# Performance work log

Hardware: AMD Instinct MI355X
Metric: run time of the kernel (lower is better)

The kernel has to match this reference:

```python
import jax, jax.numpy as jnp
import numpy as np

B, P, T = 32, 196, 32           # batch, num pixels (14*14), seq_len
E, H, A, V = 512, 512, 256, 30000  # embed, hidden, attention, vocab
FEAT = 2048

def _ln(x, g, b, eps=1e-5):
    m = jnp.mean(x, -1, keepdims=True)
    v = jnp.mean((x - m) ** 2, -1, keepdims=True)
    return (x - m) / jnp.sqrt(v + eps) * g + b

def setup_inputs() -> dict:
    key = jax.random.key(0)
    ks = iter(jax.random.split(key, 32))
    def rn(shape, s=0.05):
        return (jax.random.normal(next(ks), shape, dtype=jnp.float32) * s)
    inp = {
        'features': jax.random.normal(next(ks), (B, P, FEAT), dtype=jnp.float32),
        'captions': jax.random.randint(next(ks), (B, T), 0, V),
        # feature adapter Linear(2048->E) + LayerNorm
        'Wad': rn((E, FEAT)), 'bad': jnp.zeros((E,), jnp.float32),
        'g_ad': jnp.ones((E,), jnp.float32), 'b_ad': jnp.zeros((E,), jnp.float32),
        # additive attention
        'We': rn((A, E)), 'be': jnp.zeros((A,), jnp.float32),
        'Wd': rn((A, H)), 'bd': jnp.zeros((A,), jnp.float32),
        'Wf': rn((1, A)), 'bf': jnp.zeros((1,), jnp.float32),
        # embedding table (uniform(-0.1,0.1) as in torch init)
        'emb': jax.random.uniform(next(ks), (V, E), jnp.float32, -0.1, 0.1),
        # LSTM layer 0: input 2E, layer 1: input H; gates order i,f,g,o; forget bias 1
        'W_ih0': rn((4 * H, 2 * E)), 'W_hh0': rn((4 * H, H)),
        'b_ih0': jnp.concatenate([jnp.zeros(H), jnp.ones(H), jnp.zeros(2 * H)]).astype(jnp.float32),
        'b_hh0': jnp.zeros((4 * H,), jnp.float32),
        'W_ih1': rn((4 * H, H)), 'W_hh1': rn((4 * H, H)),
        'b_ih1': jnp.concatenate([jnp.zeros(H), jnp.ones(H), jnp.zeros(2 * H)]).astype(jnp.float32),
        'b_hh1': jnp.zeros((4 * H,), jnp.float32),
        # output head
        'W1': rn((H // 2, H)), 'b1': jnp.zeros((H // 2,), jnp.float32),
        'g1': jnp.ones((H // 2,), jnp.float32), 'bb1': jnp.zeros((H // 2,), jnp.float32),
        'W2': rn((V, H // 2)), 'b2': jnp.zeros((V,), jnp.float32),
    }
    return inp

def reference(features, captions, Wad, bad, g_ad, b_ad, We, be, Wd, bd, Wf, bf,
              emb, W_ih0, W_hh0, b_ih0, b_hh0, W_ih1, W_hh1, b_ih1, b_hh1,
              W1, b1, g1, bb1, W2, b2):
    # feature adapter (dropout = identity in eval)
    enc = _ln(jax.nn.relu(features @ Wad.T + bad), g_ad, b_ad)   # [B,P,E]
    att1 = enc @ We.T + be                                        # [B,P,A] (same every step)
    embs = emb[captions]                                          # [B,T,E]

    def lstm_cell(x, h, c, Wih, Whh, bih, bhh):
        gates = x @ Wih.T + bih + h @ Whh.T + bhh                 # [B,4H]
        i, f, g, o = jnp.split(gates, 4, axis=1)
        c_n = jax.nn.sigmoid(f) * c + jax.nn.sigmoid(i) * jnp.tanh(g)
        h_n = jax.nn.sigmoid(o) * jnp.tanh(c_n)
        return h_n, c_n

    def step(carry, emb_t):
        h, c = carry                                              # each [2,B,H]
        # additive attention against top-layer hidden state
        att2 = h[1] @ Wd.T + bd                                   # [B,A]
        e = (jax.nn.relu(att1 + att2[:, None, :]) @ Wf.T + bf)[..., 0]  # [B,P]
        alpha = jax.nn.softmax(e, axis=1)                         # (max-subtract is folded in)
        ctx = jnp.einsum('bp,bpe->be', alpha, enc)                # [B,E]
        x = jnp.concatenate([emb_t, ctx], axis=1)                 # [B,2E]
        h0, c0 = lstm_cell(x,  h[0], c[0], W_ih0, W_hh0, b_ih0, b_hh0)
        h1, c1 = lstm_cell(h0, h[1], c[1], W_ih1, W_hh1, b_ih1, b_hh1)
        out = jax.nn.relu(_ln(h1 @ W1.T + b1, g1, bb1))
        out = jnp.clip(out @ W2.T + b2, -10.0, 10.0)              # [B,V]
        return (jnp.stack([h0, h1]), jnp.stack([c0, c1])), out

    h0 = jnp.zeros((2, B, H), jnp.float32)
    c0 = jnp.zeros((2, B, H), jnp.float32)
    _, outs = jax.lax.scan(step, (h0, c0), jnp.swapaxes(embs, 0, 1))
    return jnp.swapaxes(outs, 0, 1)                               # [B,T,V]
```

## Files before the change

kernel.cpp:

```cpp
#include <hip/hip_runtime.h>

#define B_ 32
#define P_ 196
#define T_ 32
#define E_ 512
#define H_ 512
#define A_ 256
#define V_ 30000
#define FEAT_ 2048

typedef unsigned short u16;
typedef __attribute__((ext_vector_type(8))) short bf16x8;
typedef __attribute__((ext_vector_type(4))) float fx4;

#define MFMA16 __builtin_amdgcn_mfma_f32_16x16x32_bf16

__device__ __forceinline__ u16 f2b(float f){
  unsigned u = __builtin_bit_cast(unsigned, f);
  u += 0x7FFFu + ((u >> 16) & 1u);
  return (u16)(u >> 16);
}
__device__ __forceinline__ float b2f(u16 h){
  unsigned u = ((unsigned)h) << 16;
  return __builtin_bit_cast(float, u);
}
__device__ __forceinline__ float sigm(float x){ return 1.f/(1.f + __expf(-x)); }

__global__ void k_convert(const float* __restrict__ src, u16* __restrict__ dst, int n8){
  int i = blockIdx.x*256 + threadIdx.x;
  if (i >= n8) return;
  const float4* s = (const float4*)src + (size_t)i*2;
  float4 a = s[0], b = s[1];
  ushort4* d = (ushort4*)dst + (size_t)i*2;
  d[0] = make_ushort4(f2b(a.x), f2b(a.y), f2b(a.z), f2b(a.w));
  d[1] = make_ushort4(f2b(b.x), f2b(b.y), f2b(b.z), f2b(b.w));
}

__global__ void k_gather(const float* __restrict__ emb, const int* __restrict__ cap,
                         u16* __restrict__ dst){
  int r = blockIdx.x, l = threadIdx.x;
  int t = r >> 5, b = r & 31;
  int c = cap[b*T_ + t];
  const float4* s = (const float4*)(emb + (size_t)c*E_) + l*2;
  float4 a = s[0], bb = s[1];
  ushort4* d = (ushort4*)(dst + (size_t)r*E_) + l*2;
  d[0] = make_ushort4(f2b(a.x), f2b(a.y), f2b(a.z), f2b(a.w));
  d[1] = make_ushort4(f2b(bb.x), f2b(bb.y), f2b(bb.z), f2b(bb.w));
}

__global__ void k_pack_wd2(const float* __restrict__ Wd, unsigned* __restrict__ dst){
  int i = blockIdx.x*256 + threadIdx.x;
  if (i >= 256*256) return;
  int n = i & 255, kp = i >> 8;
  unsigned lo = f2b(Wd[n*512 + 2*kp]);
  unsigned hi = f2b(Wd[n*512 + 2*kp + 1]);
  dst[i] = lo | (hi << 16);
}

__global__ void k_pack_g0(const float* __restrict__ Wih, const float* __restrict__ Whh,
                          u16* __restrict__ dst){
  int eid = blockIdx.x*256 + threadIdx.x;
  if (eid >= 6144*512) return;
  int j = eid & 7, l = (eid >> 3) & 63, frag = eid >> 9;
  int ks = frag % 12; int rest = frag / 12;
  int kw = rest & 3, q = (rest >> 2) & 3, s = rest >> 4;
  int n = q*512 + s*16 + (l & 15);
  int k = kw*384 + ks*32 + ((l >> 4) << 3) + j;
  float v = (k < 1024) ? Wih[(size_t)n*1024 + k] : Whh[(size_t)n*512 + (k - 1024)];
  dst[eid] = f2b(v);
}

__global__ void k_pack_w1p(const float* __restrict__ Wih, const float* __restrict__ Whh,
                           u16* __restrict__ dst){
  int eid = blockIdx.x*256 + threadIdx.x;
  if (eid >= 32*128*512) return;
  int j = eid & 7, l = (eid >> 3) & 63, f = eid >> 9;
  int nf = f & 127, s = f >> 7;
  int np = nf*16 + (l & 15);
  int k = ((l >> 4) << 3) + j;
  int orig = ((np >> 4) & 3)*512 + (np >> 6)*16 + (np & 15);
  float v = (k < 16) ? Wih[(size_t)orig*512 + s*16 + k]
                     : Whh[(size_t)orig*512 + s*16 + (k - 16)];
  dst[eid] = f2b(v);
}

__global__ void k_bias_pack(const float* __restrict__ bih, const float* __restrict__ bhh,
                            float* __restrict__ dst){
  int n = blockIdx.x*256 + threadIdx.x;
  if (n >= 2048) return;
  int c = n & 15, q = (n >> 4) & 3, s = n >> 6;
  int orig = q*512 + s*16 + c;
  dst[n] = bih[orig] + bhh[orig];
}

__global__ void k_pack_w2(const float* __restrict__ W2f, u16* __restrict__ W2pk){
  int i = blockIdx.x*256 + threadIdx.x;
  if (i >= 960000) return;
  int l = i & 63, kc = (i >> 6) & 7, nf = i >> 9;
  int row = nf*16 + (l & 15);
  int col = kc*32 + (l >> 4)*8;
  const float4* s = (const float4*)(W2f + (size_t)row*256 + col);
  float4 a = s[0], b = s[1];
  ushort4* d = (ushort4*)(W2pk + (size_t)i*8);
  d[0] = make_ushort4(f2b(a.x), f2b(a.y), f2b(a.z), f2b(a.w));
  d[1] = make_ushort4(f2b(b.x), f2b(b.y), f2b(b.z), f2b(b.w));
}

template<int MODE, int BM, int BN, int KS>
__launch_bounds__(256)
__global__ void k_gemm(const u16* __restrict__ A, const u16* __restrict__ W,
                       const float* __restrict__ bias, u16* __restrict__ outB,
                       int M, int N, int K){
  constexpr int NI = BN/32, MI = BM/32, SEGS = KS/8;
  __shared__ __align__(16) u16 As[BM][KS+8];
  __shared__ __align__(16) u16 Bs[BN][KS+8];
  int tid = threadIdx.x;
  int l = tid & 63, w = tid >> 6;
  int wr = w >> 1, wc = w & 1;
  int m0 = blockIdx.y * BM, n0 = blockIdx.x * BN;
  fx4 acc[MI][NI];
  #pragma unroll
  for (int i=0;i<MI;i++)
    #pragma unroll
    for (int j=0;j<NI;j++) acc[i][j] = (fx4){0.f,0.f,0.f,0.f};
  int lr = l & 15, lg = l >> 4;
  for (int k0 = 0; k0 < K; k0 += KS){
    #pragma unroll
    for (int it=0; it<BM*SEGS/256; ++it){
      int flat = it*256 + tid, rr = flat/SEGS, cs = (flat%SEGS)*8;
      *(uint4*)&As[rr][cs] = *(const uint4*)(A + (size_t)(m0+rr)*K + k0 + cs);
    }
    uint4 z = {0u,0u,0u,0u};
    #pragma unroll
    for (int it=0; it<BN*SEGS/256; ++it){
      int flat = it*256 + tid, rr = flat/SEGS, cs = (flat%SEGS)*8;
      int rb = n0 + rr;
      *(uint4*)&Bs[rr][cs] = (rb < N) ? *(const uint4*)(W + (size_t)rb*K + k0 + cs) : z;
    }
    __syncthreads();
    #pragma unroll
    for (int kk=0; kk<KS/32; ++kk){
      bf16x8 av[MI], bv[NI];
      #pragma unroll
      for (int mi=0; mi<MI; mi++) av[mi] = *(const bf16x8*)&As[wr*(BM/2) + mi*16 + lr][kk*32 + lg*8];
      #pragma unroll
      for (int ni=0; ni<NI; ni++) bv[ni] = *(const bf16x8*)&Bs[wc*(BN/2) + ni*16 + lr][kk*32 + lg*8];
      #pragma unroll
      for (int mi=0; mi<MI; mi++)
        #pragma unroll
        for (int ni=0; ni<NI; ni++)
          acc[mi][ni] = MFMA16(av[mi], bv[ni], acc[mi][ni], 0, 0, 0);
    }
    __syncthreads();
  }
  #pragma unroll
  for (int mi=0; mi<MI; mi++)
    #pragma unroll
    for (int ni=0; ni<NI; ni++){
      int col = n0 + wc*(BN/2) + ni*16 + lr;
      if (col >= N) continue;
      float bvs = bias[col];
      #pragma unroll
      for (int reg=0; reg<4; reg++){
        int rowm = m0 + wr*(BM/2) + mi*16 + lg*4 + reg;
        float v = acc[mi][ni][reg] + bvs;
        if (MODE == 0) v = fmaxf(v, 0.f);
        outB[(size_t)rowm*N + col] = f2b(v);
      }
    }
}

template<int BM, int BN, int KS>
__launch_bounds__(256)
__global__ void k_gemmF(const float* __restrict__ A, const u16* __restrict__ W,
                        const float* __restrict__ bias, u16* __restrict__ outB,
                        int M, int N, int K){
  constexpr int NI = BN/32, MI = BM/32, SEGS = KS/8;
  __shared__ __align__(16) u16 As[BM][KS+8];
  __shared__ __align__(16) u16 Bs[BN][KS+8];
  int tid = threadIdx.x;
  int l = tid & 63, w = tid >> 6;
  int wr = w >> 1, wc = w & 1;
  int m0 = blockIdx.y * BM, n0 = blockIdx.x * BN;
  fx4 acc[MI][NI];
  #pragma unroll
  for (int i=0;i<MI;i++)
    #pragma unroll
    for (int j=0;j<NI;j++) acc[i][j] = (fx4){0.f,0.f,0.f,0.f};
  int lr = l & 15, lg = l >> 4;
  for (int k0 = 0; k0 < K; k0 += KS){
    #pragma unroll
    for (int it=0; it<BM*SEGS/256; ++it){
      int flat = it*256 + tid, rr = flat/SEGS, cs = (flat%SEGS)*8;
      const float4* s = (const float4*)(A + (size_t)(m0+rr)*K + k0 + cs);
      float4 a0 = s[0], a1 = s[1];
      *(ushort4*)&As[rr][cs]   = make_ushort4(f2b(a0.x), f2b(a0.y), f2b(a0.z), f2b(a0.w));
      *(ushort4*)&As[rr][cs+4] = make_ushort4(f2b(a1.x), f2b(a1.y), f2b(a1.z), f2b(a1.w));
    }
    #pragma unroll
    for (int it=0; it<BN*SEGS/256; ++it){
      int flat = it*256 + tid, rr = flat/SEGS, cs = (flat%SEGS)*8;
      *(uint4*)&Bs[rr][cs] = *(const uint4*)(W + (size_t)(n0+rr)*K + k0 + cs);
    }
    __syncthreads();
    #pragma unroll
    for (int kk=0; kk<KS/32; ++kk){
      bf16x8 av[MI], bv[NI];
      #pragma unroll
      for (int mi=0; mi<MI; mi++) av[mi] = *(const bf16x8*)&As[wr*(BM/2) + mi*16 + lr][kk*32 + lg*8];
      #pragma unroll
      for (int ni=0; ni<NI; ni++) bv[ni] = *(const bf16x8*)&Bs[wc*(BN/2) + ni*16 + lr][kk*32 + lg*8];
      #pragma unroll
      for (int mi=0; mi<MI; mi++)
        #pragma unroll
        for (int ni=0; ni<NI; ni++)
          acc[mi][ni] = MFMA16(av[mi], bv[ni], acc[mi][ni], 0, 0, 0);
    }
    __syncthreads();
  }
  #pragma unroll
  for (int mi=0; mi<MI; mi++)
    #pragma unroll
    for (int ni=0; ni<NI; ni++){
      int col = n0 + wc*(BN/2) + ni*16 + lr;
      float bvs = bias[col];
      #pragma unroll
      for (int reg=0; reg<4; reg++){
        int rowm = m0 + wr*(BM/2) + mi*16 + lg*4 + reg;
        float v = fmaxf(acc[mi][ni][reg] + bvs, 0.f);
        outB[(size_t)rowm*N + col] = f2b(v);
      }
    }
}

__global__ void k_ln1(const u16* __restrict__ pre, const float* __restrict__ g,
                      const float* __restrict__ bt, u16* __restrict__ enc){
  int row = blockIdx.x; int l = threadIdx.x;
  bf16x8 vv = *(const bf16x8*)(pre + (size_t)row*E_ + l*8);
  float x[8]; float s = 0.f;
  #pragma unroll
  for (int i=0;i<8;i++){ x[i] = b2f((u16)vv[i]); s += x[i]; }
  #pragma unroll
  for (int off=32; off; off>>=1) s += __shfl_xor(s, off, 64);
  float mean = s * (1.f/512.f);
  float vs = 0.f;
  #pragma unroll
  for (int i=0;i<8;i++){ float d = x[i]-mean; vs += d*d; }
  #pragma unroll
  for (int off=32; off; off>>=1) vs += __shfl_xor(vs, off, 64);
  float inv = rsqrtf(vs*(1.f/512.f) + 1e-5f);
  int c0 = l*8;
  u16 o[8];
  #pragma unroll
  for (int i=0;i<8;i++) o[i] = f2b((x[i]-mean)*inv*g[c0+i] + bt[c0+i]);
  ushort4* d = (ushort4*)(enc + (size_t)row*E_ + c0);
  d[0] = make_ushort4(o[0],o[1],o[2],o[3]);
  d[1] = make_ushort4(o[4],o[5],o[6],o[7]);
}

__device__ __forceinline__ void w1ln_block(const u16* __restrict__ h1all,
    const u16* __restrict__ W1, const float* __restrict__ b1,
    const float* __restrict__ g1v, const float* __restrict__ bb1,
    u16* __restrict__ hid, int u, int tid, float* red2, float* mv){
  int l = tid & 63, w = tid >> 6, lr = l & 15, lg = l >> 4;
  fx4 acc[2] = {{0,0,0,0},{0,0,0,0}};
  for (int k0 = 0; k0 < 512; k0 += 32){
    bf16x8 bv  = *(const bf16x8*)(W1 + (size_t)(w*16+lr)*512 + k0 + lg*8);
    bf16x8 av0 = *(const bf16x8*)(h1all + ((size_t)lr*T_ + u)*512 + k0 + lg*8);
    bf16x8 av1 = *(const bf16x8*)(h1all + ((size_t)(16+lr)*T_ + u)*512 + k0 + lg*8);
    acc[0] = MFMA16(av0, bv, acc[0], 0,0,0);
    acc[1] = MFMA16(av1, bv, acc[1], 0,0,0);
  }
  int col = w*16 + lr;
  float bc = b1[col];
  float val[2][4], s1[2][4], s2[2][4];
  #pragma unroll
  for (int mi=0;mi<2;mi++)
    #pragma unroll
    for (int reg=0;reg<4;reg++){
      float v = acc[mi][reg] + bc;
      val[mi][reg] = v; s1[mi][reg] = v; s2[mi][reg] = v*v;
    }
  #pragma unroll
  for (int off=1; off<16; off<<=1){
    #pragma unroll
    for (int mi=0;mi<2;mi++)
      #pragma unroll
      for (int reg=0;reg<4;reg++){
        s1[mi][reg] += __shfl_xor(s1[mi][reg], off, 64);
        s2[mi][reg] += __shfl_xor(s2[mi][reg], off, 64);
      }
  }
  if (lr == 0){
    #pragma unroll
    for (int mi=0;mi<2;mi++)
      #pragma unroll
      for (int reg=0;reg<4;reg++){
        int row = mi*16 + lg*4 + reg;
        red2[(0*16 + w)*32 + row] = s1[mi][reg];
        red2[(16   + w)*32 + row] = s2[mi][reg];
      }
  }
  __syncthreads();
  if (tid < 64){
    int which = tid >> 5, row = tid & 31;
    float s = 0.f;
    #pragma unroll
    for (int ww=0; ww<16; ++ww) s += red2[(which*16 + ww)*32 + row];
    mv[which*32 + row] = s;
  }
  __syncthreads();
  #pragma unroll
  for (int mi=0;mi<2;mi++)
    #pragma unroll
    for (int reg=0;reg<4;reg++){
      int row = mi*16 + lg*4 + reg;
      float mean = mv[row] * (1.f/256.f);
      float var  = mv[32+row] * (1.f/256.f) - mean*mean;
      float inv  = rsqrtf(var + 1e-5f);
      float o = fmaxf((val[mi][reg]-mean)*inv*g1v[col] + bb1[col], 0.f);
      hid[((size_t)u*32 + row)*256 + col] = f2b(o);
    }
}

__launch_bounds__(1024)
__global__ void k_w1(const u16* __restrict__ h1all, const u16* __restrict__ W1_16,
                     const float* __restrict__ b1, const float* __restrict__ g1v,
                     const float* __restrict__ bb1, u16* __restrict__ hid16){
  __shared__ float red2[1024];
  __shared__ float mv[64];
  w1ln_block(h1all, W1_16, b1, g1v, bb1, hid16, blockIdx.x, threadIdx.x, red2, mv);
}

__launch_bounds__(1024)
__global__ void k_head(const u16* __restrict__ hid, const u16* __restrict__ W2pk,
                       const float* __restrict__ b2, float* __restrict__ out){
  __shared__ __align__(16) union { u16 hA[32][264]; float Cs[32][260]; } S;
  int c = blockIdx.x, uh = blockIdx.y, tid = threadIdx.x;
  int l = tid & 63, w = tid >> 6, lr = l & 15, lg = l >> 4;
  int nf = c*16 + w;
  bool valid = nf < 1875;
  bf16x8 bw[8];
  if (valid){
    const u16* wp = W2pk + (size_t)nf*4096 + l*8;
    #pragma unroll
    for (int k0=0;k0<8;k0++) bw[k0] = *(const bf16x8*)(wp + k0*512);
  }
  int srow = tid >> 5, scc = (tid & 31)*8;
  int col0 = c*256 + scc;
  float bb[8];
  #pragma unroll
  for (int j=0;j<8;j++) bb[j] = (col0 + j < V_) ? b2[col0 + j] : 0.f;

  for (int ui=0; ui<16; ++ui){
    int u = uh*16 + ui;
    { int arow = tid >> 5, ak = (tid & 31)*8;
      *(uint4*)&S.hA[arow][ak] = *(const uint4*)(hid + ((size_t)u*32 + arow)*256 + ak); }
    __syncthreads();
    fx4 acc0 = {0,0,0,0}, acc1 = {0,0,0,0};
    if (valid){
      #pragma unroll
      for (int k0=0;k0<8;k0++){
        bf16x8 av0 = *(const bf16x8*)&S.hA[lr][k0*32 + lg*8];
        bf16x8 av1 = *(const bf16x8*)&S.hA[16+lr][k0*32 + lg*8];
        acc0 = MFMA16(av0, bw[k0], acc0, 0,0,0);
        acc1 = MFMA16(av1, bw[k0], acc1, 0,0,0);
      }
    }
    __syncthreads();
    #pragma unroll
    for (int reg=0; reg<4; ++reg){
      S.Cs[lg*4+reg][w*16+lr]    = acc0[reg];
      S.Cs[16+lg*4+reg][w*16+lr] = acc1[reg];
    }
    __syncthreads();
    if (col0 + 8 <= V_){
      float4 v0, v1;
      v0.x = fminf(fmaxf(S.Cs[srow][scc+0] + bb[0], -10.f), 10.f);
      v0.y = fminf(fmaxf(S.Cs[srow][scc+1] + bb[1], -10.f), 10.f);
      v0.z = fminf(fmaxf(S.Cs[srow][scc+2] + bb[2], -10.f), 10.f);
      v0.w = fminf(fmaxf(S.Cs[srow][scc+3] + bb[3], -10.f), 10.f);
      v1.x = fminf(fmaxf(S.Cs[srow][scc+4] + bb[4], -10.f), 10.f);
      v1.y = fminf(fmaxf(S.Cs[srow][scc+5] + bb[5], -10.f), 10.f);
      v1.z = fminf(fmaxf(S.Cs[srow][scc+6] + bb[6], -10.f), 10.f);
      v1.w = fminf(fmaxf(S.Cs[srow][scc+7] + bb[7], -10.f), 10.f);
      float* o = out + ((size_t)srow*T_ + u)*V_ + col0;
      *(float4*)o = v0; *(float4*)(o+4) = v1;
    }
    __syncthreads();
  }
}

__launch_bounds__(1024)
__global__ void k_ly(const float* __restrict__ part1, const float* __restrict__ bias1p,
                     float* __restrict__ c1buf, u16* __restrict__ h1all,
                     const unsigned* __restrict__ Wd2, const float* __restrict__ bd,
                     const u16* __restrict__ att1b, const u16* __restrict__ enc16,
                     const float* __restrict__ Wf, const float* __restrict__ bfp,
                     const u16* __restrict__ embs, u16* __restrict__ xh0cur, int t){
  int b = blockIdx.x, tid = threadIdx.x;
  int l = tid & 63, wid = tid >> 6;
  __shared__ float g1s[2048];
  __shared__ float h1s[512];
  __shared__ float a2p[4][256];
  __shared__ float a2[256], ev[256], red[8], wfv[256], bdv[256];
  __shared__ float cb[4][256][2];
  if (tid < 256){ wfv[tid] = Wf[tid]; bdv[tid] = bd[tid]; }
  float bf0 = bfp[0];

  if (t > 0){
    float acc0 = bias1p[tid], acc1 = bias1p[tid + 1024];
    #pragma unroll 4
    for (int s2=0; s2<32; ++s2){
      const float* pp = part1 + ((size_t)(s2*32 + b))*2048;
      acc0 += pp[tid];
      acc1 += pp[tid + 1024];
    }
    g1s[tid] = acc0; g1s[tid + 1024] = acc1;
    __syncthreads();
    if (tid < 512){
      int h = tid, s4 = h >> 4, c = h & 15, base = s4*64 + c;
      float gi = g1s[base], gf = g1s[base+16], gg = g1s[base+32], go = g1s[base+48];
      float cold = c1buf[b*512 + h];
      float cn = sigm(gf)*cold + sigm(gi)*tanhf(gg);
      c1buf[b*512 + h] = cn;
      float hn = sigm(go)*tanhf(cn);
      h1s[h] = hn;
      h1all[((size_t)b*T_ + (t-1))*512 + h] = f2b(hn);
    }
  } else {
    if (tid < 512) h1s[tid] = 0.f;
  }
  __syncthreads();
  if (t >= T_) return;

  {
    int n = tid & 255, kq = tid >> 8;
    float acc = 0.f;
    const unsigned* wp = Wd2 + (size_t)kq*64*256 + n;
    #pragma unroll 8
    for (int kp2 = 0; kp2 < 64; ++kp2){
      unsigned wv = wp[(size_t)kp2*256];
      int k0 = (kq*64 + kp2)*2;
      acc += h1s[k0]   * b2f((u16)(wv & 0xFFFFu))
           + h1s[k0+1] * b2f((u16)(wv >> 16));
    }
    a2p[kq][n] = acc;
  }
  __syncthreads();
  if (tid < 256) a2[tid] = a2p[0][tid] + a2p[1][tid] + a2p[2][tid] + a2p[3][tid] + bdv[tid];
  __syncthreads();
  for (int pi = 0; pi < 13; ++pi){
    int p = pi*16 + wid;
    if (p < P_){
      ushort4 av4 = *(const ushort4*)(att1b + (size_t)(b*P_ + p)*A_ + l*4);
      int j0 = l*4;
      float sum = fmaxf(b2f(av4.x)+a2[j0],  0.f)*wfv[j0]
                + fmaxf(b2f(av4.y)+a2[j0+1],0.f)*wfv[j0+1]
                + fmaxf(b2f(av4.z)+a2[j0+2],0.f)*wfv[j0+2]
                + fmaxf(b2f(av4.w)+a2[j0+3],0.f)*wfv[j0+3];
      #pragma unroll
      for (int off=32; off; off>>=1) sum += __shfl_xor(sum, off, 64);
      if (l == 0) ev[p] = sum + bf0;
    }
  }
  __syncthreads();
  if (tid < 256){
    float v = (tid < P_) ? ev[tid] : -1e30f;
    float m = v;
    #pragma unroll
    for (int off=32; off; off>>=1) m = fmaxf(m, __shfl_xor(m, off, 64));
    if (l == 0) red[wid] = m;
  }
  __syncthreads();
  float mg = fmaxf(fmaxf(red[0],red[1]), fmaxf(red[2],red[3]));
  if (tid < 256){
    float ex = (tid < P_) ? __expf(ev[tid] - mg) : 0.f;
    float ss = ex;
    #pragma unroll
    for (int off=32; off; off>>=1) ss += __shfl_xor(ss, off, 64);
    if (l == 0) red[4+wid] = ss;
    ev[tid] = ex;
  }
  __syncthreads();
  float inv = 1.f/(red[4]+red[5]+red[6]+red[7]);
  {
    int j = tid & 255, pq = tid >> 8;
    float A0 = 0.f, A1 = 0.f;
    const unsigned* ep = (const unsigned*)enc16 + ((size_t)b*P_ + pq*49)*256 + j;
    #pragma unroll 7
    for (int pi = 0; pi < 49; ++pi){
      unsigned vv = ep[(size_t)pi*256];
      float al = ev[pq*49 + pi];
      A0 += al * b2f((u16)(vv & 0xFFFFu));
      A1 += al * b2f((u16)(vv >> 16));
    }
    cb[pq][j][0] = A0; cb[pq][j][1] = A1;
  }
  __syncthreads();
  if (tid < 256){
    float c0 = (cb[0][tid][0]+cb[1][tid][0]+cb[2][tid][0]+cb[3][tid][0]) * inv;
    float c1 = (cb[0][tid][1]+cb[1][tid][1]+cb[2][tid][1]+cb[3][tid][1]) * inv;
    unsigned o = (unsigned)f2b(c0) | (((unsigned)f2b(c1)) << 16);
    *((unsigned*)(xh0cur + (size_t)b*1536 + 512) + tid) = o;
    ((unsigned*)(xh0cur + (size_t)b*1536))[tid] =
        ((const unsigned*)(embs + (size_t)(t*32+b)*E_))[tid];
  }
}

__launch_bounds__(1024)
__global__ void k_lx(const u16* __restrict__ xh0cur, u16* __restrict__ xh0nxt,
                     const u16* __restrict__ Wg0pk, const float* __restrict__ bias0p,
                     const u16* __restrict__ W1ppk, const u16* __restrict__ h1all,
                     float* __restrict__ c0buf, float* __restrict__ part1, int t){
  __shared__ float part[16][32][16];
  __shared__ float gsum[4][32][16];
  __shared__ __align__(16) u16 As[32][40];
  int tid = threadIdx.x, s = blockIdx.x;
  int l = tid & 63, kw = tid >> 6, lr = l & 15, lg = l >> 4;

  bf16x8 a[2][3];
  #pragma unroll
  for (int mi=0;mi<2;mi++)
    #pragma unroll
    for (int ks=0;ks<3;ks++)
      a[mi][ks] = *(const bf16x8*)(xh0cur + (size_t)(mi*16+lr)*1536 + kw*96 + ks*32 + lg*8);
  for (int q=0;q<4;q++){
    fx4 acc0 = (fx4){0,0,0,0}, acc1 = (fx4){0,0,0,0};
    const u16* wp = Wg0pk + (size_t)(((s*4+q)*4 + (kw>>2))*12 + (kw&3)*3)*512 + l*8;
    #pragma unroll
    for (int ks=0;ks<3;ks++){
      bf16x8 bf8 = *(const bf16x8*)(wp + ks*512);
      acc0 = MFMA16(a[0][ks], bf8, acc0, 0,0,0);
      acc1 = MFMA16(a[1][ks], bf8, acc1, 0,0,0);
    }
    #pragma unroll
    for (int reg=0;reg<4;reg++){
      part[kw][lg*4+reg][lr]    = acc0[reg];
      part[kw][16+lg*4+reg][lr] = acc1[reg];
    }
    __syncthreads();
    if (tid < 512){
      int bb = tid >> 4, c = tid & 15;
      float g = bias0p[s*64 + q*16 + c];
      #pragma unroll
      for (int kw2=0; kw2<16; ++kw2) g += part[kw2][bb][c];
      gsum[q][bb][c] = g;
    }
    __syncthreads();
  }
  if (tid < 256){
    int bb = tid >> 3, kk = (tid & 7)*2;
    unsigned hv = 0;
    if (t > 0) hv = *(const unsigned*)(h1all + ((size_t)bb*T_ + (t-1))*512 + s*16 + kk);
    *(unsigned*)&As[bb][16+kk] = hv;
  }
  if (tid < 512){
    int bb = tid >> 4, c = tid & 15;
    int h = s*16 + c;
    float gi = gsum[0][bb][c], gf = gsum[1][bb][c], gg = gsum[2][bb][c], go = gsum[3][bb][c];
    float cold = c0buf[bb*512 + h];
    float cn = sigm(gf)*cold + sigm(gi)*tanhf(gg);
    c0buf[bb*512 + h] = cn;
    u16 hb = f2b(sigm(go)*tanhf(cn));
    xh0nxt[(size_t)bb*1536 + 1024 + h] = hb;
    As[bb][c] = hb;
  }
  __syncthreads();
  bf16x8 pa0 = *(const bf16x8*)&As[lr][lg*8];
  bf16x8 pa1 = *(const bf16x8*)&As[16+lr][lg*8];
  #pragma unroll 2
  for (int i=0;i<8;i++){
    int nf = kw*8 + i;
    bf16x8 bf8 = *(const bf16x8*)(W1ppk + (size_t)(s*128 + nf)*512 + l*8);
    fx4 A0 = MFMA16(pa0, bf8, (fx4){0,0,0,0}, 0,0,0);
    fx4 A1 = MFMA16(pa1, bf8, (fx4){0,0,0,0}, 0,0,0);
    float* o = part1 + ((size_t)s*32)*2048 + nf*16 + lr;
    #pragma unroll
    for (int reg=0;reg<4;reg++){
      o[(size_t)(lg*4+reg)*2048]    = A0[reg];
      o[(size_t)(16+lg*4+reg)*2048] = A1[reg];
    }
  }
}

extern "C" void kernel_launch(void* const* d_in, const int* in_sizes, int n_in,
                              void* d_out, int out_size, void* d_ws, size_t ws_size,
                              hipStream_t stream){
  (void)in_sizes; (void)n_in; (void)out_size; (void)ws_size;
  const float* features = (const float*)d_in[0];
  const int*   captions = (const int*)d_in[1];
  const float* Wad  = (const float*)d_in[2];
  const float* bad  = (const float*)d_in[3];
  const float* g_ad = (const float*)d_in[4];
  const float* b_ad = (const float*)d_in[5];
  const float* We   = (const float*)d_in[6];
  const float* be   = (const float*)d_in[7];
  const float* Wd   = (const float*)d_in[8];
  const float* bd   = (const float*)d_in[9];
  const float* Wf   = (const float*)d_in[10];
  const float* bfp  = (const float*)d_in[11];
  const float* emb  = (const float*)d_in[12];
  const float* W_ih0 = (const float*)d_in[13];
  const float* W_hh0 = (const float*)d_in[14];
  const float* b_ih0 = (const float*)d_in[15];
  const float* b_hh0 = (const float*)d_in[16];
  const float* W_ih1 = (const float*)d_in[17];
  const float* W_hh1 = (const float*)d_in[18];
  const float* b_ih1 = (const float*)d_in[19];
  const float* b_hh1 = (const float*)d_in[20];
  const float* W1  = (const float*)d_in[21];
  const float* b1  = (const float*)d_in[22];
  const float* g1  = (const float*)d_in[23];
  const float* bb1 = (const float*)d_in[24];
  const float* W2  = (const float*)d_in[25];
  const float* b2  = (const float*)d_in[26];
  float* out = (float*)d_out;

  char* wsb = (char*)d_ws;
  size_t off = 0;
  auto alloc = [&](size_t bytes)->char*{
    char* p = wsb + off; off += (bytes + 255) & ~(size_t)255; return p;
  };
  u16* Wad16   = (u16*)alloc((size_t)512*2048*2);
  u16* We16    = (u16*)alloc((size_t)256*512*2);
  u16* W1_16   = (u16*)alloc((size_t)256*512*2);
  u16* W2pk    = (u16*)alloc((size_t)1875*8*512*2);
  unsigned* Wd2 = (unsigned*)alloc((size_t)256*256*4);
  u16* Wg0pk   = (u16*)alloc((size_t)2048*1536*2);
  u16* W1ppk   = (u16*)alloc((size_t)32*128*512*2);
  float* bias0p = (float*)alloc(2048*4);
  float* bias1p = (float*)alloc(2048*4);
  u16* embs16  = (u16*)alloc((size_t)1024*512*2);
  u16* pre16   = (u16*)alloc((size_t)6272*512*2);
  u16* enc16   = (u16*)alloc((size_t)6272*512*2);
  u16* att1_16 = (u16*)alloc((size_t)6272*256*2);
  u16* xh0     = (u16*)alloc((size_t)2*32*1536*2);
  float* c0buf = (float*)alloc(32*512*4);
  float* c1buf = (float*)alloc(32*512*4);
  float* part1 = (float*)alloc((size_t)32*32*2048*4);
  u16* h1all16 = (u16*)alloc((size_t)1024*512*2);
  u16* hid16   = (u16*)alloc((size_t)1024*256*2);

  auto cdiv = [](int a, int b){ return (a+b-1)/b; };

  hipMemsetAsync(xh0, 0, 196608 + 65536 + 65536, stream);

  k_convert<<<cdiv(512*2048/8,256),256,0,stream>>>(Wad, Wad16, 512*2048/8);
  k_convert<<<cdiv(256*512/8,256),256,0,stream>>>(We, We16, 256*512/8);
  k_convert<<<cdiv(256*512/8,256),256,0,stream>>>(W1, W1_16, 256*512/8);
  k_pack_w2<<<cdiv(960000,256),256,0,stream>>>(W2, W2pk);
  k_pack_wd2<<<cdiv(256*256,256),256,0,stream>>>(Wd, Wd2);
  k_pack_g0<<<cdiv(6144*512,256),256,0,stream>>>(W_ih0, W_hh0, Wg0pk);
  k_pack_w1p<<<cdiv(32*128*512,256),256,0,stream>>>(W_ih1, W_hh1, W1ppk);
  k_bias_pack<<<8,256,0,stream>>>(b_ih0, b_hh0, bias0p);
  k_bias_pack<<<8,256,0,stream>>>(b_ih1, b_hh1, bias1p);
  k_gather<<<1024,64,0,stream>>>(emb, captions, embs16);

  k_gemmF<64,64,64><<<dim3(8,98),256,0,stream>>>(features, Wad16, bad, pre16, 6272, 512, 2048);
  k_ln1<<<6272,64,0,stream>>>(pre16, g_ad, b_ad, enc16);
  k_gemm<1,64,64,64><<<dim3(4,98),256,0,stream>>>(enc16, We16, be, att1_16, 6272, 256, 512);

  u16* xb[2] = { xh0, xh0 + 32*1536 };
  for (int t = 0; t < T_; ++t){
    k_ly<<<32,1024,0,stream>>>(part1, bias1p, c1buf, h1all16, Wd2, bd,
                               att1_16, enc16, Wf, bfp, embs16, xb[t&1], t);
    k_lx<<<32,1024,0,stream>>>(xb[t&1], xb[1-(t&1)], Wg0pk, bias0p,
                               W1ppk, h1all16, c0buf, part1, t);
  }
  k_ly<<<32,1024,0,stream>>>(part1, bias1p, c1buf, h1all16, Wd2, bd,
                             att1_16, enc16, Wf, bfp, embs16, xb[0], T_);

  k_w1<<<32,1024,0,stream>>>(h1all16, W1_16, b1, g1, bb1, hid16);
  k_head<<<dim3(118,2),1024,0,stream>>>(hid16, W2pk, b2, out);
}
```

Measured before the change: 1.367 ms.

## Merge prep kernels, swizzle GEMM block order, restructure layer-0 gate reduction

```diff
diff --git a/kernel.cpp b/kernel.cpp
--- a/kernel.cpp
+++ b/kernel.cpp
@@ -26,87 +26,100 @@
 }
 __device__ __forceinline__ float sigm(float x){ return 1.f/(1.f + __expf(-x)); }
 
-__global__ void k_convert(const float* __restrict__ src, u16* __restrict__ dst, int n8){
-  int i = blockIdx.x*256 + threadIdx.x;
-  if (i >= n8) return;
-  const float4* s = (const float4*)src + (size_t)i*2;
-  float4 a = s[0], b = s[1];
-  ushort4* d = (ushort4*)dst + (size_t)i*2;
-  d[0] = make_ushort4(f2b(a.x), f2b(a.y), f2b(a.z), f2b(a.w));
-  d[1] = make_ushort4(f2b(b.x), f2b(b.y), f2b(b.z), f2b(b.w));
-}
-
-__global__ void k_gather(const float* __restrict__ emb, const int* __restrict__ cap,
-                         u16* __restrict__ dst){
-  int r = blockIdx.x, l = threadIdx.x;
-  int t = r >> 5, b = r & 31;
-  int c = cap[b*T_ + t];
-  const float4* s = (const float4*)(emb + (size_t)c*E_) + l*2;
-  float4 a = s[0], bb = s[1];
-  ushort4* d = (ushort4*)(dst + (size_t)r*E_) + l*2;
-  d[0] = make_ushort4(f2b(a.x), f2b(a.y), f2b(a.z), f2b(a.w));
-  d[1] = make_ushort4(f2b(bb.x), f2b(bb.y), f2b(bb.z), f2b(bb.w));
-}
-
-__global__ void k_pack_wd2(const float* __restrict__ Wd, unsigned* __restrict__ dst){
-  int i = blockIdx.x*256 + threadIdx.x;
-  if (i >= 256*256) return;
-  int n = i & 255, kp = i >> 8;
-  unsigned lo = f2b(Wd[n*512 + 2*kp]);
-  unsigned hi = f2b(Wd[n*512 + 2*kp + 1]);
-  dst[i] = lo | (hi << 16);
-}
-
-__global__ void k_pack_g0(const float* __restrict__ Wih, const float* __restrict__ Whh,
-                          u16* __restrict__ dst){
-  int eid = blockIdx.x*256 + threadIdx.x;
-  if (eid >= 6144*512) return;
-  int j = eid & 7, l = (eid >> 3) & 63, frag = eid >> 9;
-  int ks = frag % 12; int rest = frag / 12;
-  int kw = rest & 3, q = (rest >> 2) & 3, s = rest >> 4;
-  int n = q*512 + s*16 + (l & 15);
-  int k = kw*384 + ks*32 + ((l >> 4) << 3) + j;
-  float v = (k < 1024) ? Wih[(size_t)n*1024 + k] : Whh[(size_t)n*512 + (k - 1024)];
-  dst[eid] = f2b(v);
-}
-
-__global__ void k_pack_w1p(const float* __restrict__ Wih, const float* __restrict__ Whh,
-                           u16* __restrict__ dst){
-  int eid = blockIdx.x*256 + threadIdx.x;
-  if (eid >= 32*128*512) return;
-  int j = eid & 7, l = (eid >> 3) & 63, f = eid >> 9;
-  int nf = f & 127, s = f >> 7;
-  int np = nf*16 + (l & 15);
-  int k = ((l >> 4) << 3) + j;
-  int orig = ((np >> 4) & 3)*512 + (np >> 6)*16 + (np & 15);
-  float v = (k < 16) ? Wih[(size_t)orig*512 + s*16 + k]
-                     : Whh[(size_t)orig*512 + s*16 + (k - 16)];
-  dst[eid] = f2b(v);
-}
-
-__global__ void k_bias_pack(const float* __restrict__ bih, const float* __restrict__ bhh,
-                            float* __restrict__ dst){
-  int n = blockIdx.x*256 + threadIdx.x;
-  if (n >= 2048) return;
-  int c = n & 15, q = (n >> 4) & 3, s = n >> 6;
-  int orig = q*512 + s*16 + c;
-  dst[n] = bih[orig] + bhh[orig];
-}
-
-__global__ void k_pack_w2(const float* __restrict__ W2f, u16* __restrict__ W2pk){
-  int i = blockIdx.x*256 + threadIdx.x;
-  if (i >= 960000) return;
-  int l = i & 63, kc = (i >> 6) & 7, nf = i >> 9;
-  int row = nf*16 + (l & 15);
-  int col = kc*32 + (l >> 4)*8;
-  const float4* s = (const float4*)(W2f + (size_t)row*256 + col);
-  float4 a = s[0], b = s[1];
-  ushort4* d = (ushort4*)(W2pk + (size_t)i*8);
-  d[0] = make_ushort4(f2b(a.x), f2b(a.y), f2b(a.z), f2b(a.w));
-  d[1] = make_ushort4(f2b(b.x), f2b(b.y), f2b(b.z), f2b(b.w));
-}
-
-template<int MODE, int BM, int BN, int KS>
+#define PREP_BLOCKS 25398
+__global__ void k_prep(const float* __restrict__ Wad, const float* __restrict__ We,
+                       const float* __restrict__ W1f, const float* __restrict__ W2f,
+                       const float* __restrict__ Wd,
+                       const float* __restrict__ Wih0, const float* __restrict__ Whh0,
+                       const float* __restrict__ Wih1, const float* __restrict__ Whh1,
+                       const float* __restrict__ bih0, const float* __restrict__ bhh0,
+                       const float* __restrict__ bih1, const float* __restrict__ bhh1,
+                       const float* __restrict__ emb, const int* __restrict__ cap,
+                       u16* __restrict__ Wad16, u16* __restrict__ We16,
+                       u16* __restrict__ W1_16, u16* __restrict__ W2pk,
+                       unsigned* __restrict__ Wd2, u16* __restrict__ Wg0pk,
+                       u16* __restrict__ W1ppk, float* __restrict__ bias0p,
+                       float* __restrict__ bias1p, u16* __restrict__ embs16){
+  int bid = blockIdx.x, tid = threadIdx.x;
+  if (bid < 12288){
+    int eid = bid*256 + tid;
+    int j = eid & 7, l = (eid >> 3) & 63, frag = eid >> 9;
+    int ks = frag % 12; int rest = frag / 12;
+    int kw = rest & 3, q = (rest >> 2) & 3, s = rest >> 4;
+    int n = q*512 + s*16 + (l & 15);
+    int k = kw*384 + ks*32 + ((l >> 4) << 3) + j;
+    float v = (k < 1024) ? Wih0[(size_t)n*1024 + k] : Whh0[(size_t)n*512 + (k - 1024)];
+    Wg0pk[eid] = f2b(v);
+  } else if (bid < 20480){
+    int eid = (bid-12288)*256 + tid;
+    int j = eid & 7, l = (eid >> 3) & 63, f = eid >> 9;
+    int nf = f & 127, s = f >> 7;
+    int np = nf*16 + (l & 15);
+    int k = ((l >> 4) << 3) + j;
+    int orig = ((np >> 4) & 3)*512 + (np >> 6)*16 + (np & 15);
+    float v = (k < 16) ? Wih1[(size_t)orig*512 + s*16 + k]
+                       : Whh1[(size_t)orig*512 + s*16 + (k - 16)];
+    W1ppk[eid] = f2b(v);
+  } else if (bid < 24230){
+    int i = (bid-20480)*256 + tid;
+    int l = i & 63, kc = (i >> 6) & 7, nf = i >> 9;
+    int row = nf*16 + (l & 15);
+    int col = kc*32 + (l >> 4)*8;
+    const float4* s = (const float4*)(W2f + (size_t)row*256 + col);
+    float4 a = s[0], b = s[1];
+    ushort4* d = (ushort4*)(W2pk + (size_t)i*8);
+    d[0] = make_ushort4(f2b(a.x), f2b(a.y), f2b(a.z), f2b(a.w));
+    d[1] = make_ushort4(f2b(b.x), f2b(b.y), f2b(b.z), f2b(b.w));
+  } else if (bid < 24742){
+    int i = (bid-24230)*256 + tid;
+    const float4* s = (const float4*)Wad + (size_t)i*2;
+    float4 a = s[0], b = s[1];
+    ushort4* d = (ushort4*)Wad16 + (size_t)i*2;
+    d[0] = make_ushort4(f2b(a.x), f2b(a.y), f2b(a.z), f2b(a.w));
+    d[1] = make_ushort4(f2b(b.x), f2b(b.y), f2b(b.z), f2b(b.w));
+  } else if (bid < 24806){
+    int i = (bid-24742)*256 + tid;
+    const float4* s = (const float4*)We + (size_t)i*2;
+    float4 a = s[0], b = s[1];
+    ushort4* d = (ushort4*)We16 + (size_t)i*2;
+    d[0] = make_ushort4(f2b(a.x), f2b(a.y), f2b(a.z), f2b(a.w));
+    d[1] = make_ushort4(f2b(b.x), f2b(b.y), f2b(b.z), f2b(b.w));
+  } else if (bid < 24870){
+    int i = (bid-24806)*256 + tid;
+    const float4* s = (const float4*)W1f + (size_t)i*2;
+    float4 a = s[0], b = s[1];
+    ushort4* d = (ushort4*)W1_16 + (size_t)i*2;
+    d[0] = make_ushort4(f2b(a.x), f2b(a.y), f2b(a.z), f2b(a.w));
+    d[1] = make_ushort4(f2b(b.x), f2b(b.y), f2b(b.z), f2b(b.w));
+  } else if (bid < 25126){
+    int i = (bid-24870)*256 + tid;
+    int n = i & 255, kp = i >> 8;
+    unsigned lo = f2b(Wd[n*512 + 2*kp]);
+    unsigned hi = f2b(Wd[n*512 + 2*kp + 1]);
+    Wd2[i] = lo | (hi << 16);
+  } else if (bid < 25134){
+    int n = (bid-25126)*256 + tid;
+    int c = n & 15, q = (n >> 4) & 3, s = n >> 6;
+    int orig = q*512 + s*16 + c;
+    bias0p[n] = bih0[orig] + bhh0[orig];
+  } else if (bid < 25142){
+    int n = (bid-25134)*256 + tid;
+    int c = n & 15, q = (n >> 4) & 3, s = n >> 6;
+    int orig = q*512 + s*16 + c;
+    bias1p[n] = bih1[orig] + bhh1[orig];
+  } else {
+    int r = (bid-25142)*4 + (tid >> 6), l = tid & 63;
+    int t = r >> 5, b = r & 31;
+    int c = cap[b*T_ + t];
+    const float4* s = (const float4*)(emb + (size_t)c*E_) + l*2;
+    float4 a = s[0], bb = s[1];
+    ushort4* d = (ushort4*)(embs16 + (size_t)r*E_) + l*2;
+    d[0] = make_ushort4(f2b(a.x), f2b(a.y), f2b(a.z), f2b(a.w));
+    d[1] = make_ushort4(f2b(bb.x), f2b(bb.y), f2b(bb.z), f2b(bb.w));
+  }
+}
+
+template<int MODE, int BM, int BN, int KS, int NQ>
 __launch_bounds__(256)
 __global__ void k_gemm(const u16* __restrict__ A, const u16* __restrict__ W,
                        const float* __restrict__ bias, u16* __restrict__ outB,
@@ -114,10 +127,15 @@
   constexpr int NI = BN/32, MI = BM/32, SEGS = KS/8;
   __shared__ __align__(16) u16 As[BM][KS+8];
   __shared__ __align__(16) u16 Bs[BN][KS+8];
+  int f = blockIdx.x;
+  int p8 = f & 7; int rest = f >> 3;
+  int q = rest % NQ; int pHigh = rest / NQ;
+  int p = pHigh*8 + p8;
+  if (p*BM >= M) return;
+  int m0 = p*BM, n0 = q*BN;
   int tid = threadIdx.x;
   int l = tid & 63, w = tid >> 6;
   int wr = w >> 1, wc = w & 1;
-  int m0 = blockIdx.y * BM, n0 = blockIdx.x * BN;
   fx4 acc[MI][NI];
   #pragma unroll
   for (int i=0;i<MI;i++)
@@ -170,7 +188,7 @@
     }
 }
 
-template<int BM, int BN, int KS>
+template<int BM, int BN, int KS, int NQ>
 __launch_bounds__(256)
 __global__ void k_gemmF(const float* __restrict__ A, const u16* __restrict__ W,
                         const float* __restrict__ bias, u16* __restrict__ outB,
@@ -178,10 +196,15 @@
   constexpr int NI = BN/32, MI = BM/32, SEGS = KS/8;
   __shared__ __align__(16) u16 As[BM][KS+8];
   __shared__ __align__(16) u16 Bs[BN][KS+8];
+  int f = blockIdx.x;
+  int p8 = f & 7; int rest = f >> 3;
+  int q = rest % NQ; int pHigh = rest / NQ;
+  int p = pHigh*8 + p8;
+  if (p*BM >= M) return;
+  int m0 = p*BM, n0 = q*BN;
   int tid = threadIdx.x;
   int l = tid & 63, w = tid >> 6;
   int wr = w >> 1, wc = w & 1;
-  int m0 = blockIdx.y * BM, n0 = blockIdx.x * BN;
   fx4 acc[MI][NI];
   #pragma unroll
   for (int i=0;i<MI;i++)
@@ -513,48 +536,53 @@
                      const u16* __restrict__ Wg0pk, const float* __restrict__ bias0p,
                      const u16* __restrict__ W1ppk, const u16* __restrict__ h1all,
                      float* __restrict__ c0buf, float* __restrict__ part1, int t){
-  __shared__ float part[16][32][16];
+  __shared__ float part4[4][4][32][16];
   __shared__ float gsum[4][32][16];
   __shared__ __align__(16) u16 As[32][40];
   int tid = threadIdx.x, s = blockIdx.x;
   int l = tid & 63, kw = tid >> 6, lr = l & 15, lg = l >> 4;
-
-  bf16x8 a[2][3];
-  #pragma unroll
-  for (int mi=0;mi<2;mi++)
-    #pragma unroll
-    for (int ks=0;ks<3;ks++)
-      a[mi][ks] = *(const bf16x8*)(xh0cur + (size_t)(mi*16+lr)*1536 + kw*96 + ks*32 + lg*8);
-  for (int q=0;q<4;q++){
-    fx4 acc0 = (fx4){0,0,0,0}, acc1 = (fx4){0,0,0,0};
-    const u16* wp = Wg0pk + (size_t)(((s*4+q)*4 + (kw>>2))*12 + (kw&3)*3)*512 + l*8;
-    #pragma unroll
-    for (int ks=0;ks<3;ks++){
-      bf16x8 bf8 = *(const bf16x8*)(wp + ks*512);
-      acc0 = MFMA16(a[0][ks], bf8, acc0, 0,0,0);
-      acc1 = MFMA16(a[1][ks], bf8, acc1, 0,0,0);
-    }
-    #pragma unroll
-    for (int reg=0;reg<4;reg++){
-      part[kw][lg*4+reg][lr]    = acc0[reg];
-      part[kw][16+lg*4+reg][lr] = acc1[reg];
-    }
-    __syncthreads();
-    if (tid < 512){
-      int bb = tid >> 4, c = tid & 15;
-      float g = bias0p[s*64 + q*16 + c];
-      #pragma unroll
-      for (int kw2=0; kw2<16; ++kw2) g += part[kw2][bb][c];
-      gsum[q][bb][c] = g;
-    }
-    __syncthreads();
-  }
+  int q = kw >> 2, kw4 = kw & 3;
+
   if (tid < 256){
     int bb = tid >> 3, kk = (tid & 7)*2;
     unsigned hv = 0;
     if (t > 0) hv = *(const unsigned*)(h1all + ((size_t)bb*T_ + (t-1))*512 + s*16 + kk);
     *(unsigned*)&As[bb][16+kk] = hv;
   }
+
+  fx4 acc0 = (fx4){0,0,0,0}, acc1 = (fx4){0,0,0,0};
+  const u16* wp = Wg0pk + (size_t)(((s*4+q)*4 + kw4)*12)*512 + l*8;
+  #pragma unroll
+  for (int half=0; half<2; ++half){
+    bf16x8 a0[6], a1[6];
+    #pragma unroll
+    for (int ks=0; ks<6; ++ks){
+      int k = kw4*384 + (half*6+ks)*32 + lg*8;
+      a0[ks] = *(const bf16x8*)(xh0cur + (size_t)lr*1536 + k);
+      a1[ks] = *(const bf16x8*)(xh0cur + (size_t)(16+lr)*1536 + k);
+    }
+    #pragma unroll
+    for (int ks=0; ks<6; ++ks){
+      bf16x8 bf8 = *(const bf16x8*)(wp + (half*6+ks)*512);
+      acc0 = MFMA16(a0[ks], bf8, acc0, 0,0,0);
+      acc1 = MFMA16(a1[ks], bf8, acc1, 0,0,0);
+    }
+  }
+  #pragma unroll
+  for (int reg=0;reg<4;reg++){
+    part4[q][kw4][lg*4+reg][lr]    = acc0[reg];
+    part4[q][kw4][16+lg*4+reg][lr] = acc1[reg];
+  }
+  __syncthreads();
+  #pragma unroll
+  for (int pp=0; pp<2; ++pp){
+    int pid = tid + pp*1024;
+    int q2 = pid >> 9, bb = (pid >> 4) & 31, c = pid & 15;
+    gsum[q2][bb][c] = part4[q2][0][bb][c] + part4[q2][1][bb][c]
+                    + part4[q2][2][bb][c] + part4[q2][3][bb][c]
+                    + bias0p[s*64 + q2*16 + c];
+  }
+  __syncthreads();
   if (tid < 512){
     int bb = tid >> 4, c = tid & 15;
     int h = s*16 + c;
@@ -642,24 +670,18 @@
   u16* h1all16 = (u16*)alloc((size_t)1024*512*2);
   u16* hid16   = (u16*)alloc((size_t)1024*256*2);
 
-  auto cdiv = [](int a, int b){ return (a+b-1)/b; };
-
   hipMemsetAsync(xh0, 0, 196608 + 65536 + 65536, stream);
 
-  k_convert<<<cdiv(512*2048/8,256),256,0,stream>>>(Wad, Wad16, 512*2048/8);
-  k_convert<<<cdiv(256*512/8,256),256,0,stream>>>(We, We16, 256*512/8);
-  k_convert<<<cdiv(256*512/8,256),256,0,stream>>>(W1, W1_16, 256*512/8);
-  k_pack_w2<<<cdiv(960000,256),256,0,stream>>>(W2, W2pk);
-  k_pack_wd2<<<cdiv(256*256,256),256,0,stream>>>(Wd, Wd2);
-  k_pack_g0<<<cdiv(6144*512,256),256,0,stream>>>(W_ih0, W_hh0, Wg0pk);
-  k_pack_w1p<<<cdiv(32*128*512,256),256,0,stream>>>(W_ih1, W_hh1, W1ppk);
-  k_bias_pack<<<8,256,0,stream>>>(b_ih0, b_hh0, bias0p);
-  k_bias_pack<<<8,256,0,stream>>>(b_ih1, b_hh1, bias1p);
-  k_gather<<<1024,64,0,stream>>>(emb, captions, embs16);
-
-  k_gemmF<64,64,64><<<dim3(8,98),256,0,stream>>>(features, Wad16, bad, pre16, 6272, 512, 2048);
+  k_prep<<<PREP_BLOCKS,256,0,stream>>>(Wad, We, W1, W2, Wd,
+                                       W_ih0, W_hh0, W_ih1, W_hh1,
+                                       b_ih0, b_hh0, b_ih1, b_hh1,
+                                       emb, captions,
+                                       Wad16, We16, W1_16, W2pk, Wd2,
+                                       Wg0pk, W1ppk, bias0p, bias1p, embs16);
+
+  k_gemmF<64,64,64,8><<<832,256,0,stream>>>(features, Wad16, bad, pre16, 6272, 512, 2048);
   k_ln1<<<6272,64,0,stream>>>(pre16, g_ad, b_ad, enc16);
-  k_gemm<1,64,64,64><<<dim3(4,98),256,0,stream>>>(enc16, We16, be, att1_16, 6272, 256, 512);
+  k_gemm<1,64,64,64,4><<<416,256,0,stream>>>(enc16, We16, be, att1_16, 6272, 256, 512);
 
   u16* xb[2] = { xh0, xh0 + 32*1536 };
   for (int t = 0; t < T_; ++t){
```

Measured after the change: 1.509 ms. 10.3% more time.
